# Performance work log

Measured on AMD Instinct MI355X. Metric: run time of the kernel, lower is better.

## Reference

```python
import jax, jax.numpy as jnp
import numpy as np


def _hemisphere(radius=1.0, n=5):
    # replicates DiffuseShader.generate_hemisphere with sample=(5j,5j)
    u, v = np.mgrid[0:np.pi:n * 1j, 0:np.pi:n * 1j]
    x = (radius * np.cos(u) * np.sin(v)).flatten()
    y = (radius * np.sin(u) * np.sin(v)).flatten()
    z = (radius * np.cos(v)).flatten()
    return jnp.asarray(np.c_[x, y, z], dtype=jnp.float32)


def _diffuse_forward(V, COL, OPA, p, l, normals, hemi_vecs, indices, pointindex):
    P, S, N = p.shape[0], hemi_vecs.shape[0], V.shape[0]
    local = pointindex % P
    # --- project_hemisphere_projection: Rodrigues rotation local->global ---
    u = l[None, :] - p                                      # [P,3]
    u_hat = u / jnp.linalg.norm(u, axis=1, keepdims=True)
    v_loc = jnp.broadcast_to(jnp.array([0.0, -1.0, 0.0], p.dtype), u_hat.shape)
    c = -u_hat[:, 1:2]                                      # rowwise dot(v_loc, u_hat), [P,1]
    w = jnp.cross(v_loc, u_hat)                             # [P,3]
    z0 = jnp.zeros_like(w[:, 0])
    vmat = jnp.stack([jnp.stack([z0, -w[:, 2], w[:, 1]], -1),
                      jnp.stack([w[:, 2], z0, -w[:, 0]], -1),
                      jnp.stack([-w[:, 1], w[:, 0], z0], -1)], axis=1)  # [P,3,3] skew(w)
    R = jnp.eye(3, dtype=p.dtype)[None] + vmat + jnp.matmul(vmat, vmat) / (1.0 + c)[..., None]
    lh = jnp.einsum('pij,sj->psi', R, hemi_vecs) + l        # [P,S,3]
    o = jnp.broadcast_to(p[:, None, :], (P, S, 3))
    d = lh - o
    # --- get_intersection: ray/plane distances ---
    nrm = jnp.cross(V[:, 1] - V[:, 0], V[:, 2] - V[:, 0])
    nrm = nrm / jnp.linalg.norm(nrm, axis=1, keepdims=True)  # [N,3]
    kk = -jnp.sum(nrm * V[:, 3], axis=1)                     # [N]
    vo = o.reshape(P * S, 3) @ nrm.T                         # [P*S,N]
    vd = d.reshape(P * S, 3) @ nrm.T
    t = (-(kk[None, :] + vo) / vd).reshape(P, N, S)          # faithful to torch .view(P,N,S) on the [P*S,N] buffer
    surf = indices[pointindex, 0]
    mat = indices[pointindex, 1]
    empty = jnp.zeros((P, N, S), bool).at[local, surf, :].set(True)
    viable = (t > -1e-4) & (t < 1.0) & (~empty)
    # --- barycentric condition test ---
    r = o[:, None, :, :] + t[..., None] * d[:, None, :, :]   # [P,N,S,3]
    a0 = V[:, 0, 0][None, :, None]; a1 = V[:, 0, 1][None, :, None]; a2 = V[:, 0, 2][None, :, None]
    b0 = V[:, 1, 0][None, :, None]; b1 = V[:, 1, 1][None, :, None]; b2 = V[:, 1, 2][None, :, None]
    c0 = V[:, 2, 0][None, :, None]; c1 = V[:, 2, 1][None, :, None]; c2 = V[:, 2, 2][None, :, None]
    r0, r1, r2 = r[..., 0], r[..., 1], r[..., 2]
    A = a0 * r2 - a2 * r0
    B = a0 * b2 - a2 * b0
    C = a0 * r1 - a1 * r0
    D = a0 * b1 - a1 * b0
    E = a0 * c2 - a2 * c0
    F = B * (a1 * c0 - a0 * c1)
    gam = (D * (A * D - B * C)) / (D * (E * D + F))
    beta = (C + gam * (a1 * c0 - a0 * c1)) / D
    alpha = (r0 - (beta * b0 + gam * c0)) / a0
    mask = jnp.where(viable & (beta > 0.0) & (gam > 0.0) & (alpha > 0.0), 1.0, 0.0).astype(jnp.float32)
    col = COL[surf, mat]                                     # [P,3]
    opa = jnp.clip(OPA[surf, mat], 0.0, 1.0)                 # [P]
    reflected_ray = l[None, :] - p                           # [P,3]
    return mask, col, opa, reflected_ray


def setup_inputs() -> dict:
    P, N, M, G = 512, 1024, 8, 2048
    key = jax.random.key(0)
    ks = jax.random.split(key, 8)
    V = jax.random.normal(ks[0], (N, 4, 3), jnp.float32)
    indices = jax.random.randint(ks[1], (G, 2), 0, M)
    pointindex = jax.random.randint(ks[2], (P,), 0, G)
    COL = jax.random.uniform(ks[3], (N, M, 3), jnp.float32)
    OPA = jax.random.uniform(ks[4], (N, M), jnp.float32)
    p = jax.random.normal(ks[5], (P, 3), jnp.float32) * 5.0
    l = jax.random.normal(ks[6], (3,), jnp.float32) * 10.0 + 20.0
    normals = jax.random.normal(ks[7], (N, 3), jnp.float32)
    return {"V": V, "indices": indices, "pointindex": pointindex, "COL": COL,
            "OPA": OPA, "p": p, "l": l, "normals": normals, "it": 0,
            "hemi_vecs": _hemisphere(1.0, 5)}


def reference(V, indices, pointindex, COL, OPA, p, l, normals, it, hemi_vecs):
    return _diffuse_forward(V, COL, OPA, p, l, normals, hemi_vecs, indices, pointindex)
```

## Files before the change

### kernel.cpp

```cpp
#include <hip/hip_runtime.h>
#include <math.h>

#define NP   512
#define NT   1024
#define NS   25
#define NPS  (NP*NS)
#define MASKN (NP*NT*NS)

#define DSA_OFF  0
#define PD_OFF   51200
#define NX_OFF   53248
#define NY_OFF   54272
#define NZ_OFF   55296
#define KK_OFF   56320
#define W_OFF    57344
#define EMPTY_OFF ((size_t)67584 * 8)

__device__ __forceinline__ double sgn(double x) {
    return (x > 0.0) ? 1.0 : ((x < 0.0) ? -1.0 : 0.0);
}

__global__ void prep_all(const float* __restrict__ p,
                         const float* __restrict__ l,
                         const float* __restrict__ hemi,
                         const float* __restrict__ V,
                         const int* __restrict__ indices,
                         const int* __restrict__ pointindex,
                         const float* __restrict__ COL,
                         const float* __restrict__ OPA,
                         double* __restrict__ ws,
                         unsigned* __restrict__ emptyMask,
                         float* __restrict__ out) {
    const int b = blockIdx.x, t = threadIdx.x;
    if (b < 50) {
        int idx = b * 256 + t;
        int pi = idx / NS, si = idx % NS;
        double px = p[pi*3+0], py = p[pi*3+1], pz = p[pi*3+2];
        double lx = l[0], ly = l[1], lz = l[2];
        double ux = lx - px, uy = ly - py, uz = lz - pz;
        double nrm = sqrt(ux*ux + uy*uy + uz*uz);
        ux /= nrm; uy /= nrm; uz /= nrm;
        double c = -uy;
        double wx = -uz, wz = ux;
        double m01 = -wz, m10 = wz, m12 = -wx, m21 = wx;
        double q00 = m01*m10;
        double q02 = m01*m12;
        double q11 = m10*m01 + m12*m21;
        double q20 = m21*m10;
        double q22 = m21*m12;
        double ic = 1.0 + c;
        double r00 = 1.0 + q00/ic, r01 = m01,            r02 = q02/ic;
        double r10 = m10,          r11 = 1.0 + q11/ic,   r12 = m12;
        double r20 = q20/ic,       r21 = m21,            r22 = 1.0 + q22/ic;
        double hx = hemi[si*3+0], hy = hemi[si*3+1], hz = hemi[si*3+2];
        double lhx = r00*hx + r01*hy + r02*hz + lx;
        double lhy = r10*hx + r11*hy + r12*hz + ly;
        double lhz = r20*hx + r21*hy + r22*hz + lz;
        double* dsA = ws + DSA_OFF;
        dsA[idx*4+0] = lhx - px;
        dsA[idx*4+1] = lhy - py;
        dsA[idx*4+2] = lhz - pz;
        dsA[idx*4+3] = 0.0;
    } else if (b < 54) {
        int n = (b - 50) * 256 + t;
        const float* v = V + n*12;
        double a0=v[0], a1=v[1], a2=v[2];
        double b0=v[3], b1=v[4], b2=v[5];
        double c0=v[6], c1=v[7], c2=v[8];
        double v3x=v[9], v3y=v[10], v3z=v[11];
        double e1x=b0-a0, e1y=b1-a1, e1z=b2-a2;
        double e2x=c0-a0, e2y=c1-a1, e2z=c2-a2;
        double cx = e1y*e2z - e1z*e2y;
        double cy = e1z*e2x - e1x*e2z;
        double cz = e1x*e2y - e1y*e2x;
        double nn = sqrt(cx*cx + cy*cy + cz*cz);
        double nx = cx/nn, ny = cy/nn, nz = cz/nn;
        double kk = -(nx*v3x + ny*v3y + nz*v3z);
        double Bv = a0*b2 - a2*b0;
        double Dv = a0*b1 - a1*b0;
        double Ec = a0*c2 - a2*c0;
        double G2 = a1*c0 - a0*c1;
        double Fc = Bv*G2;
        double gd = Dv*(Ec*Dv + Fc);
        double gq = Dv*gd;
        double dq = Dv*c0;
        double aq = a0*gq;
        double WGr0 = a1*Bv - a2*Dv, WGr1 = -(a0*Bv), WGr2 = a0*Dv;
        double dg = Dv*G2;
        double WBr0 = -(a1*gd) + dg*WGr0;
        double WBr1 =  a0*gd  + dg*WGr1;
        double WBr2 =            dg*WGr2;
        double dd = Dv*dq;
        double WAr0 = gq - b0*WBr0 - dd*WGr0;
        double WAr1 =    - b0*WBr1 - dd*WGr1;
        double WAr2 =    - b0*WBr2 - dd*WGr2;
        double sg = sgn(Dv*gd), sb = sgn(gq), sa = sgn(aq);
        ws[NX_OFF + n] = nx;
        ws[NY_OFF + n] = ny;
        ws[NZ_OFF + n] = nz;
        ws[KK_OFF + n] = kk;
        double* W = ws + W_OFF + n*10;
        W[0] = WGr0*sg; W[1] = WGr1*sg; W[2] = WGr2*sg;
        W[3] = WBr0*sb; W[4] = WBr1*sb; W[5] = WBr2*sb;
        W[6] = WAr0*sa; W[7] = WAr1*sa; W[8] = WAr2*sa;
        W[9] = 0.0;
    } else {
        emptyMask[t] = 0u;
        emptyMask[t + 256] = 0u;
        __syncthreads();
        for (int i = t; i < NP; i += 256) {
            int pidx = pointindex[i];
            int local = pidx & (NP - 1);
            int surf = indices[pidx*2 + 0];
            int mat  = indices[pidx*2 + 1];
            atomicOr(&emptyMask[local], 1u << surf);
            float* colOut = out + MASKN;
            float* opaOut = out + MASKN + 3*NP;
            float* refOut = out + MASKN + 4*NP;
            colOut[i*3+0] = COL[(surf*8+mat)*3+0];
            colOut[i*3+1] = COL[(surf*8+mat)*3+1];
            colOut[i*3+2] = COL[(surf*8+mat)*3+2];
            float o = OPA[surf*8+mat];
            opaOut[i] = fminf(fmaxf(o, 0.0f), 1.0f);
            refOut[i*3+0] = (float)((double)l[0] - (double)p[i*3+0]);
            refOut[i*3+1] = (float)((double)l[1] - (double)p[i*3+1]);
            refOut[i*3+2] = (float)((double)l[2] - (double)p[i*3+2]);
            double* pd = ws + PD_OFF;
            pd[i*4+0] = (double)p[i*3+0];
            pd[i*4+1] = (double)p[i*3+1];
            pd[i*4+2] = (double)p[i*3+2];
            pd[i*4+3] = 0.0;
        }
    }
}

template<bool HE>
__device__ __forceinline__ void line_body(
        const double* __restrict__ ws, const double (*sW)[11],
        const double* sdx, const double* sdy, const double* sdz,
        double sx, double sy, double sz, double ox, double oy, double oz,
        unsigned em, unsigned nn0, unsigned q, unsigned ps, unsigned tid,
        float* __restrict__ out) {
    const unsigned n0 = tid * 4u;
    const double2 nxa = *(const double2*)(ws + NX_OFF + n0);
    const double2 nxb = *(const double2*)(ws + NX_OFF + n0 + 2);
    const double2 nya = *(const double2*)(ws + NY_OFF + n0);
    const double2 nyb = *(const double2*)(ws + NY_OFF + n0 + 2);
    const double2 nza = *(const double2*)(ws + NZ_OFF + n0);
    const double2 nzb = *(const double2*)(ws + NZ_OFF + n0 + 2);
    const double2 kka = *(const double2*)(ws + KK_OFF + n0);
    const double2 kkb = *(const double2*)(ws + KK_OFF + n0 + 2);

    const unsigned rem0 = (q << 10) + n0;
    unsigned nn = rem0 / 25u;
    unsigned ss = rem0 - nn * 25u;

    float res[4];
    #pragma unroll
    for (int k = 0; k < 4; ++k) {
        const double nxv = (k < 2) ? (k ? nxa.y : nxa.x) : (k == 3 ? nxb.y : nxb.x);
        const double nyv = (k < 2) ? (k ? nya.y : nya.x) : (k == 3 ? nyb.y : nyb.x);
        const double nzv = (k < 2) ? (k ? nza.y : nza.x) : (k == 3 ? nzb.y : nzb.x);
        const double kkv = (k < 2) ? (k ? kka.y : kka.x) : (k == 3 ? kkb.y : kkb.x);

        const double vd = fma(sz, nzv, fma(sy, nyv, sx * nxv));
        const double tt = fma(oz, nzv, fma(oy, nyv, fma(ox, nxv, kkv)));
        const double e1 = fma(1e-4, vd, -tt);
        const double e2 = vd + tt;

        const double dxv = sdx[ss], dyv = sdy[ss], dzv = sdz[ss];
        const double R0 = fma(-tt, dxv, vd * ox);
        const double R1 = fma(-tt, dyv, vd * oy);
        const double R2 = fma(-tt, dzv, vd * oz);

        const double* w = sW[nn - nn0];
        const double dG = fma(R2, w[2], fma(R1, w[1], R0 * w[0]));
        const double dB = fma(R2, w[5], fma(R1, w[4], R0 * w[3]));
        const double dA = fma(R2, w[8], fma(R1, w[7], R0 * w[6]));

        const int hv = __double2hiint(vd);
        int m = (__double2hiint(e1) ^ hv) | (__double2hiint(e2) ^ hv)
              | (__double2hiint(dG) ^ hv) | (__double2hiint(dB) ^ hv)
              | (__double2hiint(dA) ^ hv);
        bool ok = (m >= 0);
        if (HE) ok = ok && !((nn < 8u) && ((em >> nn) & 1u));
        res[k] = ok ? 1.0f : 0.0f;

        ++ss;
        if (ss == 25u) { ss = 0u; ++nn; }
    }
    *(float4*)(out + ps*1024u + n0) = make_float4(res[0], res[1], res[2], res[3]);
}

__global__ __launch_bounds__(256) void diffuse_main(
        const double* __restrict__ ws,
        const unsigned* __restrict__ emptyMask,
        float* __restrict__ out) {
    __shared__ double sW[42][11];
    __shared__ double sdx[25], sdy[25], sdz[25];

    const unsigned ps = blockIdx.x;
    const unsigned pp = ps / 25u;
    const unsigned q  = ps - pp * 25u;
    const unsigned nn0 = (q << 10) / 25u;
    const unsigned tid = threadIdx.x;

    const double* Wg = ws + W_OFF;
    {
        unsigned i = tid;
        if (i < 210u) {
            unsigned row = i / 5u, col = i - row * 5u;
            unsigned gn = nn0 + row; if (gn > 1023u) gn = 1023u;
            const double2 v = *(const double2*)(Wg + gn*10u + col*2u);
            sW[row][col*2u]   = v.x;
            sW[row][col*2u+1] = v.y;
        }
        if (i < 25u) {
            const double* dr = ws + DSA_OFF + (pp*25u + i)*4u;
            sdx[i] = dr[0]; sdy[i] = dr[1]; sdz[i] = dr[2];
        }
    }
    const double sx = ws[DSA_OFF + ps*4u + 0];
    const double sy = ws[DSA_OFF + ps*4u + 1];
    const double sz = ws[DSA_OFF + ps*4u + 2];
    const double ox = ws[PD_OFF + pp*4u + 0];
    const double oy = ws[PD_OFF + pp*4u + 1];
    const double oz = ws[PD_OFF + pp*4u + 2];
    const unsigned em = (q == 0u) ? emptyMask[pp] : 0u;
    __syncthreads();

    if (q == 0u)
        line_body<true >(ws, sW, sdx, sdy, sdz, sx, sy, sz, ox, oy, oz,
                         em, nn0, q, ps, tid, out);
    else
        line_body<false>(ws, sW, sdx, sdy, sdz, sx, sy, sz, ox, oy, oz,
                         em, nn0, q, ps, tid, out);
}

extern "C" void kernel_launch(void* const* d_in, const int* in_sizes, int n_in,
                              void* d_out, int out_size, void* d_ws, size_t ws_size,
                              hipStream_t stream) {
    const float* V         = (const float*)d_in[0];
    const int*   indices   = (const int*)  d_in[1];
    const int*   pointindex= (const int*)  d_in[2];
    const float* COL       = (const float*)d_in[3];
    const float* OPA       = (const float*)d_in[4];
    const float* p         = (const float*)d_in[5];
    const float* l         = (const float*)d_in[6];
    const float* hemi      = (const float*)d_in[9];

    float* out = (float*)d_out;
    double* ws = (double*)d_ws;
    unsigned* emptyMask = (unsigned*)((char*)d_ws + EMPTY_OFF);

    prep_all<<<55, 256, 0, stream>>>(p, l, hemi, V, indices, pointindex,
                                     COL, OPA, ws, emptyMask, out);
    diffuse_main<<<NPS, 256, 0, stream>>>(ws, emptyMask, out);
}
```

Before: 39.90 us.

## Process five output lines per block to reuse normals and plane terms

```diff
diff --git a/kernel.cpp b/kernel.cpp
--- a/kernel.cpp
+++ b/kernel.cpp
@@ -15,6 +15,8 @@
 #define KK_OFF   56320
 #define W_OFF    57344
 #define EMPTY_OFF ((size_t)67584 * 8)
+
+#define NROWS 207
 
 __device__ __forceinline__ double sgn(double x) {
     return (x > 0.0) ? 1.0 : ((x < 0.0) ? -1.0 : 0.0);
@@ -135,11 +137,12 @@
 }
 
 template<bool HE>
-__device__ __forceinline__ void line_body(
+__device__ __forceinline__ void lines_body(
         const double* __restrict__ ws, const double (*sW)[11],
         const double* sdx, const double* sdy, const double* sdz,
-        double sx, double sy, double sz, double ox, double oy, double oz,
-        unsigned em, unsigned nn0, unsigned q, unsigned ps, unsigned tid,
+        const double (*sSv)[4],
+        double ox, double oy, double oz,
+        unsigned em, unsigned nn0, unsigned q0, unsigned pp, unsigned tid,
         float* __restrict__ out) {
     const unsigned n0 = tid * 4u;
     const double2 nxa = *(const double2*)(ws + NX_OFF + n0);
@@ -151,90 +154,109 @@
     const double2 kka = *(const double2*)(ws + KK_OFF + n0);
     const double2 kkb = *(const double2*)(ws + KK_OFF + n0 + 2);
 
-    const unsigned rem0 = (q << 10) + n0;
-    unsigned nn = rem0 / 25u;
-    unsigned ss = rem0 - nn * 25u;
-
-    float res[4];
+    double nxk[4], nyk[4], nzk[4], ttk[4];
     #pragma unroll
     for (int k = 0; k < 4; ++k) {
         const double nxv = (k < 2) ? (k ? nxa.y : nxa.x) : (k == 3 ? nxb.y : nxb.x);
         const double nyv = (k < 2) ? (k ? nya.y : nya.x) : (k == 3 ? nyb.y : nyb.x);
         const double nzv = (k < 2) ? (k ? nza.y : nza.x) : (k == 3 ? nzb.y : nzb.x);
         const double kkv = (k < 2) ? (k ? kka.y : kka.x) : (k == 3 ? kkb.y : kkb.x);
-
-        const double vd = fma(sz, nzv, fma(sy, nyv, sx * nxv));
-        const double tt = fma(oz, nzv, fma(oy, nyv, fma(ox, nxv, kkv)));
-        const double e1 = fma(1e-4, vd, -tt);
-        const double e2 = vd + tt;
-
-        const double dxv = sdx[ss], dyv = sdy[ss], dzv = sdz[ss];
-        const double R0 = fma(-tt, dxv, vd * ox);
-        const double R1 = fma(-tt, dyv, vd * oy);
-        const double R2 = fma(-tt, dzv, vd * oz);
-
-        const double* w = sW[nn - nn0];
-        const double dG = fma(R2, w[2], fma(R1, w[1], R0 * w[0]));
-        const double dB = fma(R2, w[5], fma(R1, w[4], R0 * w[3]));
-        const double dA = fma(R2, w[8], fma(R1, w[7], R0 * w[6]));
-
-        const int hv = __double2hiint(vd);
-        int m = (__double2hiint(e1) ^ hv) | (__double2hiint(e2) ^ hv)
-              | (__double2hiint(dG) ^ hv) | (__double2hiint(dB) ^ hv)
-              | (__double2hiint(dA) ^ hv);
-        bool ok = (m >= 0);
-        if (HE) ok = ok && !((nn < 8u) && ((em >> nn) & 1u));
-        res[k] = ok ? 1.0f : 0.0f;
-
-        ++ss;
-        if (ss == 25u) { ss = 0u; ++nn; }
-    }
-    *(float4*)(out + ps*1024u + n0) = make_float4(res[0], res[1], res[2], res[3]);
+        nxk[k] = nxv; nyk[k] = nyv; nzk[k] = nzv;
+        ttk[k] = fma(oz, nzv, fma(oy, nyv, fma(ox, nxv, kkv)));
+    }
+
+    #pragma unroll
+    for (int L = 0; L < 5; ++L) {
+        const double sx = sSv[L][0], sy = sSv[L][1], sz = sSv[L][2];
+        unsigned rem = ((q0 + (unsigned)L) << 10) + n0;
+        unsigned nn = rem / 25u;
+        unsigned ss = rem - nn * 25u;
+        const double* wr = sW[nn - nn0];
+        double w0 = wr[0], w1 = wr[1], w2 = wr[2];
+        double w3 = wr[3], w4 = wr[4], w5 = wr[5];
+        double w6 = wr[6], w7 = wr[7], w8 = wr[8];
+
+        float res[4];
+        #pragma unroll
+        for (int k = 0; k < 4; ++k) {
+            const double tt = ttk[k];
+            const double vd = fma(sz, nzk[k], fma(sy, nyk[k], sx * nxk[k]));
+            const double e1 = fma(1e-4, vd, -tt);
+            const double e2 = vd + tt;
+
+            const double dxv = sdx[ss], dyv = sdy[ss], dzv = sdz[ss];
+            const double R0 = fma(-tt, dxv, vd * ox);
+            const double R1 = fma(-tt, dyv, vd * oy);
+            const double R2 = fma(-tt, dzv, vd * oz);
+
+            const double dG = fma(R2, w2, fma(R1, w1, R0 * w0));
+            const double dB = fma(R2, w5, fma(R1, w4, R0 * w3));
+            const double dA = fma(R2, w8, fma(R1, w7, R0 * w6));
+
+            const int hv = __double2hiint(vd);
+            int m = (__double2hiint(e1) ^ hv) | (__double2hiint(e2) ^ hv)
+                  | (__double2hiint(dG) ^ hv) | (__double2hiint(dB) ^ hv)
+                  | (__double2hiint(dA) ^ hv);
+            bool ok = (m >= 0);
+            if (HE) ok = ok && !((nn < 8u) && ((em >> nn) & 1u));
+            res[k] = ok ? 1.0f : 0.0f;
+
+            if (k < 3) {
+                if (++ss == 25u) {
+                    ss = 0u; ++nn;
+                    const double* wn = sW[nn - nn0];
+                    w0 = wn[0]; w1 = wn[1]; w2 = wn[2];
+                    w3 = wn[3]; w4 = wn[4]; w5 = wn[5];
+                    w6 = wn[6]; w7 = wn[7]; w8 = wn[8];
+                }
+            }
+        }
+        *(float4*)(out + (((pp*25u + q0 + (unsigned)L) << 10) + n0)) =
+            make_float4(res[0], res[1], res[2], res[3]);
+    }
 }
 
 __global__ __launch_bounds__(256) void diffuse_main(
         const double* __restrict__ ws,
         const unsigned* __restrict__ emptyMask,
         float* __restrict__ out) {
-    __shared__ double sW[42][11];
+    __shared__ double sW[NROWS][11];
     __shared__ double sdx[25], sdy[25], sdz[25];
-
-    const unsigned ps = blockIdx.x;
-    const unsigned pp = ps / 25u;
-    const unsigned q  = ps - pp * 25u;
-    const unsigned nn0 = (q << 10) / 25u;
+    __shared__ double sSv[5][4];
+
+    const unsigned pp = blockIdx.x / 5u;
+    const unsigned g  = blockIdx.x - pp * 5u;
+    const unsigned q0 = g * 5u;
+    const unsigned nn0 = (q0 << 10) / 25u;
     const unsigned tid = threadIdx.x;
 
     const double* Wg = ws + W_OFF;
-    {
-        unsigned i = tid;
-        if (i < 210u) {
-            unsigned row = i / 5u, col = i - row * 5u;
-            unsigned gn = nn0 + row; if (gn > 1023u) gn = 1023u;
-            const double2 v = *(const double2*)(Wg + gn*10u + col*2u);
-            sW[row][col*2u]   = v.x;
-            sW[row][col*2u+1] = v.y;
-        }
-        if (i < 25u) {
-            const double* dr = ws + DSA_OFF + (pp*25u + i)*4u;
-            sdx[i] = dr[0]; sdy[i] = dr[1]; sdz[i] = dr[2];
-        }
-    }
-    const double sx = ws[DSA_OFF + ps*4u + 0];
-    const double sy = ws[DSA_OFF + ps*4u + 1];
-    const double sz = ws[DSA_OFF + ps*4u + 2];
+    for (unsigned i = tid; i < NROWS*5u; i += 256u) {
+        unsigned row = i / 5u, col = i - row * 5u;
+        unsigned gn = nn0 + row; if (gn > 1023u) gn = 1023u;
+        const double2 v = *(const double2*)(Wg + gn*10u + col*2u);
+        sW[row][col*2u]   = v.x;
+        sW[row][col*2u+1] = v.y;
+    }
+    if (tid < 25u) {
+        const double* dr = ws + DSA_OFF + (pp*25u + tid)*4u;
+        sdx[tid] = dr[0]; sdy[tid] = dr[1]; sdz[tid] = dr[2];
+    } else if (tid >= 32u && tid < 52u) {
+        unsigned j = tid - 32u, L = j >> 2, c = j & 3u;
+        sSv[L][c] = ws[DSA_OFF + (pp*25u + q0 + L)*4u + c];
+    }
     const double ox = ws[PD_OFF + pp*4u + 0];
     const double oy = ws[PD_OFF + pp*4u + 1];
     const double oz = ws[PD_OFF + pp*4u + 2];
-    const unsigned em = (q == 0u) ? emptyMask[pp] : 0u;
+    const unsigned em = emptyMask[pp];
     __syncthreads();
 
-    if (q == 0u)
-        line_body<true >(ws, sW, sdx, sdy, sdz, sx, sy, sz, ox, oy, oz,
-                         em, nn0, q, ps, tid, out);
+    if (g == 0u)
+        lines_body<true >(ws, sW, sdx, sdy, sdz, sSv, ox, oy, oz,
+                          em, nn0, q0, pp, tid, out);
     else
-        line_body<false>(ws, sW, sdx, sdy, sdz, sx, sy, sz, ox, oy, oz,
-                         em, nn0, q, ps, tid, out);
+        lines_body<false>(ws, sW, sdx, sdy, sdz, sSv, ox, oy, oz,
+                          em, nn0, q0, pp, tid, out);
 }
 
 extern "C" void kernel_launch(void* const* d_in, const int* in_sizes, int n_in,
@@ -255,5 +277,5 @@
 
     prep_all<<<55, 256, 0, stream>>>(p, l, hemi, V, indices, pointindex,
                                      COL, OPA, ws, emptyMask, out);
-    diffuse_main<<<NPS, 256, 0, stream>>>(ws, emptyMask, out);
-}
+    diffuse_main<<<NP*5, 256, 0, stream>>>(ws, emptyMask, out);
+}
```

Result: slower. 41.70 us (+4.5%).
